# Kernel tuning notes

Hardware: AMD Instinct MI355X
Metric: run time of the kernel (lower is better)

The kernel has to match this reference:

```python
import jax, jax.numpy as jnp
import numpy as np

EPS = 1e-5  # BatchNorm eps (torch default); BN is in training mode with gamma=1, beta=0 (init values)


def bn(x, axes):
    m = jnp.mean(x, axis=axes, keepdims=True)
    v = jnp.var(x, axis=axes, keepdims=True)
    return (x - m) * jax.lax.rsqrt(v + EPS)


def knn_idx(xyz, k):
    # brute-force squared-distance matrix [B,N,N], k smallest
    d = jnp.sum((xyz[:, :, None, :] - xyz[:, None, :, :]) ** 2, axis=-1)
    _, idx = jax.lax.top_k(-d, k)
    return idx  # [B,N,k]


def gather(x, idx):
    # x: [B,N,C], idx: [B,N,k] -> [B,N,k,C]
    return jax.vmap(lambda a, i: a[i])(x, idx)


def lse(xyz, features, idx, w):
    nbr_xyz = gather(xyz, idx)                       # [B,N,k,3]
    rel = nbr_xyz - xyz[:, :, None, :]
    dist = jnp.sqrt(jnp.maximum(jnp.sum(rel ** 2, -1, keepdims=True), 1e-12))
    nbr_f = gather(features, idx)                    # [B,N,k,C]
    enc = jnp.concatenate([rel, dist, nbr_f], -1)    # [B,N,k,C+4]
    return jax.nn.relu(bn(jnp.einsum('bnkc,oc->bnko', enc, w), (0, 1, 2)))


def att_pool(x, sw1, sw2, sb2, mw):
    # x: [B,N,k,C]
    h = jax.nn.relu(bn(jnp.einsum('bnkc,oc->bnko', x, sw1), (0, 1, 2)))
    scores = jax.nn.softmax(jnp.einsum('bnkc,oc->bnko', h, sw2) + sb2, axis=2)  # softmax over k
    feat = jnp.sum(x * scores, axis=2)               # [B,N,C]
    return jax.nn.relu(bn(jnp.einsum('bnc,oc->bno', feat, mw), (0, 1)))


def drb(x, w1, w2):
    # in_channels == out_channels -> identity shortcut
    h = jax.nn.relu(bn(jnp.einsum('bnc,oc->bno', x, w1), (0, 1)))
    h = bn(jnp.einsum('bnc,oc->bno', h, w2), (0, 1))
    return jax.nn.relu(h + x)


def setup_inputs() -> dict:
    key = jax.random.key(0)
    B, N, C, K, OUT = 4, 8192, 32, 16, 128
    H = OUT // 2  # 64
    ks = jax.random.split(key, 16)
    s = 0.05
    return {
        'xyz': jax.random.normal(ks[0], (B, N, 3), jnp.float32),
        'features': jax.random.normal(ks[1], (B, N, C), jnp.float32),
        'w_lse1': jax.random.normal(ks[2], (H, C + 4), jnp.float32) * s,
        'w_lse2': jax.random.normal(ks[3], (H, C + 4), jnp.float32) * s,
        'ap1_sw1': jax.random.normal(ks[4], (H, H), jnp.float32) * s,
        'ap1_sw2': jax.random.normal(ks[5], (1, H), jnp.float32) * s,
        'ap1_sb2': jax.random.normal(ks[6], (1,), jnp.float32) * s,
        'ap1_mw': jax.random.normal(ks[7], (H, H), jnp.float32) * s,
        'ap2_sw1': jax.random.normal(ks[8], (H, H), jnp.float32) * s,
        'ap2_sw2': jax.random.normal(ks[9], (1, H), jnp.float32) * s,
        'ap2_sb2': jax.random.normal(ks[10], (1,), jnp.float32) * s,
        'ap2_mw': jax.random.normal(ks[11], (H, H), jnp.float32) * s,
        'drb_w1': jax.random.normal(ks[12], (OUT, OUT), jnp.float32) * s,
        'drb_w2': jax.random.normal(ks[13], (OUT, OUT), jnp.float32) * s,
    }


def reference(xyz, features, w_lse1, w_lse2, ap1_sw1, ap1_sw2, ap1_sb2, ap1_mw,
              ap2_sw1, ap2_sw2, ap2_sb2, ap2_mw, drb_w1, drb_w2):
    K = 16
    idx = knn_idx(xyz, K)  # original calls knn twice on same xyz -> identical indices
    f1 = att_pool(lse(xyz, features, idx, w_lse1), ap1_sw1, ap1_sw2, ap1_sb2, ap1_mw)
    f2 = att_pool(lse(xyz, features, idx, w_lse2), ap2_sw1, ap2_sw2, ap2_sb2, ap2_mw)
    agg = jnp.concatenate([f1, f2], axis=-1)  # [B,N,128]
    return drb(agg, drb_w1, drb_w2)           # [B,N,128]
```

## Files before the change

kernel.cpp:

```cpp
#include <hip/hip_runtime.h>
#include <hip/hip_bf16.h>
#include <hip/hip_fp16.h>
#include <float.h>
#include <math.h>

#define DEVFN __device__ __forceinline__

DEVFN void wavefence() { __builtin_amdgcn_wave_barrier(); }

using half8 = __attribute__((ext_vector_type(8))) _Float16;
using f32x4 = __attribute__((ext_vector_type(4))) float;

namespace {
constexpr int Bq = 4, Nq = 8192, Cq = 32, Kq = 16;
constexpr int PTS = Bq * Nq;
constexpr int CH = 16;
constexpr int CAND = Nq / CH;
constexpr double ROWS = 524288.0;

constexpr int DS_Y = 0, DS_Z = 256, DS_G = 512, DS_H1 = 768, DS_H2 = 1024;

constexpr size_t OFF_KD   = 0;
constexpr size_t OFF_KJ   = (size_t)32 << 20;
constexpr size_t OFF_X    = 0;
constexpr size_t OFF_Z    = (size_t)64 << 20;
constexpr size_t OFF_H1   = 0;
constexpr size_t OFF_H2   = (size_t)16 << 20;
constexpr size_t OFF_GRAW = (size_t)192 << 20;
constexpr size_t OFF_AGG  = (size_t)208 << 20;
constexpr size_t OFF_IDX  = (size_t)224 << 20;
constexpr size_t OFF_DST  = (size_t)226 << 20;
constexpr size_t OFF_MST  = ((size_t)226 << 20) + 10240;
constexpr size_t OFF_BNP  = ((size_t)226 << 20) + 16384;
constexpr size_t WS_NEED  = ((size_t)226 << 20) + 32768;
constexpr size_t FB_GRAW  = (size_t)64 << 20;
constexpr size_t FB_AGG   = (size_t)80 << 20;
constexpr size_t FB_H1    = (size_t)96 << 20;
constexpr size_t FB_H2    = (size_t)112 << 20;
constexpr size_t FB_IDX   = (size_t)128 << 20;
constexpr size_t FB_DST   = (size_t)130 << 20;
constexpr size_t FB_MST   = ((size_t)130 << 20) + 10240;
constexpr size_t FB_BNP   = ((size_t)130 << 20) + 16384;
}

#define TOP16_DECL                                                           \
  float e0=FLT_MAX,e1=FLT_MAX,e2=FLT_MAX,e3=FLT_MAX,e4=FLT_MAX,e5=FLT_MAX,  \
        e6=FLT_MAX,e7=FLT_MAX,e8=FLT_MAX,e9=FLT_MAX,e10=FLT_MAX,            \
        e11=FLT_MAX,e12=FLT_MAX,e13=FLT_MAX,e14=FLT_MAX,e15=FLT_MAX;

#define PMERGE(i, im1, im2)                                                  \
  e##i = fminf(fminf(e##i, fmaxf(e##im1, b0)), fmaxf(e##im2, b1));
#define PMERGE_ALL                                                           \
  PMERGE(15,14,13) PMERGE(14,13,12) PMERGE(13,12,11) PMERGE(12,11,10)        \
  PMERGE(11,10,9) PMERGE(10,9,8) PMERGE(9,8,7) PMERGE(8,7,6) PMERGE(7,6,5)   \
  PMERGE(6,5,4) PMERGE(5,4,3) PMERGE(4,3,2) PMERGE(3,2,1) PMERGE(2,1,0)      \
  e1 = fminf(fminf(e1, fmaxf(e0, b0)), b1);                                  \
  e0 = fminf(e0, b0);

DEVFN float distf(const float4 c, const float qx, const float qy, const float qz) {
  const float dx = qx - c.x, dy = qy - c.y, dz = qz - c.z;
  return __fadd_rn(__fadd_rn(__fmul_rn(dx, dx), __fmul_rn(dy, dy)), __fmul_rn(dz, dz));
}

__global__ __launch_bounds__(256, 4) void knn_chunk_kernel(const float* __restrict__ xyz,
                                                           float* __restrict__ pd,
                                                           int* __restrict__ pj) {
  const int b = blockIdx.z;
  const int ch = blockIdx.y;
  const int n = blockIdx.x * 256 + threadIdx.x;
  __shared__ __align__(16) float4 tile[CAND];
  const float* xb = xyz + (size_t)b * Nq * 3;
  for (int t = threadIdx.x; t < CAND; t += 256) {
    const int j = ch * CAND + t;
    tile[t] = make_float4(xb[j * 3], xb[j * 3 + 1], xb[j * 3 + 2], 0.f);
  }
  __syncthreads();
  const float qx = xb[n * 3], qy = xb[n * 3 + 1], qz = xb[n * 3 + 2];
  TOP16_DECL;
  for (int t = 0; t < CAND; t += 4) {
    const float4 c0 = tile[t], c1 = tile[t + 1], c2 = tile[t + 2], c3 = tile[t + 3];
    const float u0 = distf(c0, qx, qy, qz);
    const float u1 = distf(c1, qx, qy, qz);
    const float u2 = distf(c2, qx, qy, qz);
    const float u3 = distf(c3, qx, qy, qz);
    { const float b0 = fminf(u0, u1), b1 = fmaxf(u0, u1); PMERGE_ALL }
    { const float b0 = fminf(u2, u3), b1 = fmaxf(u2, u3); PMERGE_ALL }
  }
  const float kth = e15;
  const size_t base = (((size_t)b * Nq + n) * CH + ch) * Kq;
  int cnt = 0, tfirst = -1;
  for (int t = 0; t < CAND; ++t) {
    const float d = distf(tile[t], qx, qy, qz);
    if (d < kth) { pd[base + cnt] = d; pj[base + cnt] = ch * CAND + t; ++cnt; }
    tfirst = (d == kth && tfirst < 0) ? t : tfirst;
  }
  if (cnt == 15) {
    pd[base + 15] = kth; pj[base + 15] = ch * CAND + tfirst; cnt = 16;
  }
  if (__any(cnt < 16)) {
    for (int t = 0; t < CAND; ++t) {
      const float d = distf(tile[t], qx, qy, qz);
      if (d == kth && cnt < 16) { pd[base + cnt] = d; pj[base + cnt] = ch * CAND + t; ++cnt; }
    }
  }
}

__global__ __launch_bounds__(256, 4) void knn_merge_kernel(const float* __restrict__ pd,
                                                           const int* __restrict__ pj,
                                                           int* __restrict__ idxo) {
  const int q = blockIdx.x * 256 + threadIdx.x;
  const float* dp = pd + (size_t)q * CH * Kq;
  const int* jp = pj + (size_t)q * CH * Kq;
  TOP16_DECL;
  for (int t = 0; t < CH * Kq; t += 4) {
    const float4 v = *(const float4*)(dp + t);
    { const float b0 = fminf(v.x, v.y), b1 = fmaxf(v.x, v.y); PMERGE_ALL }
    { const float b0 = fminf(v.z, v.w), b1 = fmaxf(v.z, v.w); PMERGE_ALL }
  }
  const float kth = e15;
  int* op = idxo + (size_t)q * Kq;
  int cnt = 0;
  for (int t = 0; t < CH * Kq; ++t) {
    const float d = dp[t];
    if (d < kth) { op[cnt] = jp[t]; ++cnt; }
  }
  for (int t = 0; t < CH * Kq; ++t) {
    const float d = dp[t];
    if (d == kth && cnt < 16) { op[cnt] = jp[t]; ++cnt; }
  }
}

struct PF { float4 f0, f1; float nx, ny, nz; };

DEVFN PF issue_feat(const float* __restrict__ features, const float* __restrict__ xyz,
                    int p, int j, int sub) {
  const int b = p >> 13;
  const float* fr = features + ((size_t)b * Nq + j) * Cq;
  const float* xb = xyz + ((size_t)b * Nq + j) * 3;
  PF r;
  r.f0 = *(const float4*)(fr + sub * 8);
  r.f1 = *(const float4*)(fr + sub * 8 + 4);
  r.nx = xb[0]; r.ny = xb[1]; r.nz = xb[2];
  return r;
}

DEVFN int issue_idx(const int* __restrict__ idx, int p, int lane) {
  return idx[(size_t)p * Kq + (lane >> 2)];
}

DEVFN float3 issue_query(const float* __restrict__ xyz, int p) {
  const float* q = xyz + (size_t)p * 3;
  return make_float3(q[0], q[1], q[2]);
}

DEVFN void commit_enc(__half* __restrict__ enc, int lane, const PF& pf,
                      float qx, float qy, float qz) {
  const int k = lane >> 2, sub = lane & 3;
  __half* er = enc + k * 40;
  union { float4 f; __half2 h[4]; } u;
  u.h[0] = __floats2half2_rn(pf.f0.x, pf.f0.y);
  u.h[1] = __floats2half2_rn(pf.f0.z, pf.f0.w);
  u.h[2] = __floats2half2_rn(pf.f1.x, pf.f1.y);
  u.h[3] = __floats2half2_rn(pf.f1.z, pf.f1.w);
  *(float4*)(er + sub * 8) = u.f;
  if (sub == 0) {
    const float rx = pf.nx - qx, ry = pf.ny - qy, rz = pf.nz - qz;
    const float ss = rx * rx + ry * ry + rz * rz;
    const float dd = sqrtf(fmaxf(ss, 1e-12f));
    __half2* rd = (__half2*)(er + 32);
    rd[0] = __floats2half2_rn(rx, ry);
    rd[1] = __floats2half2_rn(rz, dd);
  }
}

DEVFN void commit_enc128(__half* __restrict__ enc, int lane, const PF& pf,
                         float qx, float qy, float qz) {
  const int k = lane >> 2, sub = lane & 3;
  char* base = (char*)enc + k * 128;
  union { float4 f; __half2 h[4]; } u;
  u.h[0] = __floats2half2_rn(pf.f0.x, pf.f0.y);
  u.h[1] = __floats2half2_rn(pf.f0.z, pf.f0.w);
  u.h[2] = __floats2half2_rn(pf.f1.x, pf.f1.y);
  u.h[3] = __floats2half2_rn(pf.f1.z, pf.f1.w);
  *(float4*)(base + ((sub ^ (k & 7)) * 16)) = u.f;
  if (sub == 0) {
    const float rx = pf.nx - qx, ry = pf.ny - qy, rz = pf.nz - qz;
    const float ss = rx * rx + ry * ry + rz * rz;
    const float dd = sqrtf(fmaxf(ss, 1e-12f));
    __half2* aux = (__half2*)(base + ((4 ^ (k & 7)) * 16));
    aux[0] = __floats2half2_rn(rx, ry);
    aux[1] = __floats2half2_rn(rz, dd);
  }
}

DEVFN void zero_enc_pad(__half* __restrict__ enc, int lane) {
  if (lane < 16) {
    const __half2 z2 = __floats2half2_rn(0.f, 0.f);
    __half2* pz = (__half2*)(enc + lane * 40 + 36);
    pz[0] = z2; pz[1] = z2;
  }
}

DEVFN float dot40h(const __half* __restrict__ er, const __half2* __restrict__ wh2) {
  float a0 = 0.f, a1 = 0.f, a2 = 0.f, a3 = 0.f;
#pragma unroll
  for (int r = 0; r < 5; ++r) {
    union { float4 f; __half2 h[4]; } u;
    u.f = *(const float4*)(er + r * 8);
#pragma unroll
    for (int q = 0; q < 4; ++q) {
      const __half2 xv = u.h[q];
      const __half2 wv = wh2[r * 4 + q];
      if (q & 1) {
        a2 += __low2float(xv) * __low2float(wv);
        a3 += __high2float(xv) * __high2float(wv);
      } else {
        a0 += __low2float(xv) * __low2float(wv);
        a1 += __high2float(xv) * __high2float(wv);
      }
    }
  }
  return (a0 + a1) + (a2 + a3);
}

DEVFN float dot64x(const __half* __restrict__ xr, const __half2* __restrict__ sh2) {
  float a0 = 0.f, a1 = 0.f, a2 = 0.f, a3 = 0.f;
#pragma unroll
  for (int r = 0; r < 8; ++r) {
    union { float4 f; __half2 h[4]; } u;
    u.f = *(const float4*)(xr + r * 8);
#pragma unroll
    for (int q = 0; q < 4; ++q) {
      const __half2 xv = u.h[q];
      const __half2 wv = sh2[r * 4 + q];
      if (q & 1) {
        a2 += __low2float(xv) * __low2float(wv);
        a3 += __high2float(xv) * __high2float(wv);
      } else {
        a0 += __low2float(xv) * __low2float(wv);
        a1 += __high2float(xv) * __high2float(wv);
      }
    }
  }
  return (a0 + a1) + (a2 + a3);
}

DEVFN void load_w40(const float* __restrict__ Wrow, __half2* wh2) {
#pragma unroll
  for (int c = 0; c < 16; ++c)
    wh2[c] = __floats2half2_rn(Wrow[4 + 2 * c], Wrow[5 + 2 * c]);
  wh2[16] = __floats2half2_rn(Wrow[0], Wrow[1]);
  wh2[17] = __floats2half2_rn(Wrow[2], Wrow[3]);
  wh2[18] = __floats2half2_rn(0.f, 0.f);
  wh2[19] = wh2[18];
}

DEVFN void load_b1(const float* __restrict__ W, int lane, half8* b1) {
  const int o16 = lane & 15, q = lane >> 4;
#pragma unroll
  for (int t = 0; t < 4; ++t) {
    const int o = t * 16 + o16;
#pragma unroll
    for (int ks = 0; ks < 2; ++ks) {
      half8 v;
#pragma unroll
      for (int j = 0; j < 8; ++j) {
        const int s = ks * 32 + q * 8 + j;
        float wv = 0.f;
        if (s < 36) { const int orig = (s < 32) ? (s + 4) : (s - 32); wv = W[o * 36 + orig]; }
        v[j] = (_Float16)wv;
      }
      b1[t * 2 + ks] = v;
    }
  }
}

DEVFN void load_b2(const float* __restrict__ S1, int lane, half8* b2) {
  const int o16 = lane & 15, q = lane >> 4;
#pragma unroll
  for (int t = 0; t < 4; ++t) {
    const int o = t * 16 + o16;
#pragma unroll
    for (int ks = 0; ks < 2; ++ks) {
      half8 v;
#pragma unroll
      for (int j = 0; j < 8; ++j) {
        const int c = ks * 32 + q * 8 + j;
        v[j] = (_Float16)S1[o * 64 + c];
      }
      b2[t * 2 + ks] = v;
    }
  }
}

#define GATHER_PROLOGUE                                                      \
  int p = wid;                                                               \
  int jc = issue_idx(idx, p, lane);                                          \
  PF cur = issue_feat(features, xyz, p, jc, lane & 3);                       \
  float3 qc = issue_query(xyz, p);                                           \
  int pn0 = p + nw; if (pn0 >= PTS) pn0 = p;                                 \
  int jn = issue_idx(idx, pn0, lane);                                        \
  float3 qn = issue_query(xyz, pn0);                                         \
  for (; p < PTS; p += nw) {                                                 \
    int pn = p + nw; if (pn >= PTS) pn = p;                                  \
    int pn2 = pn + nw; if (pn2 >= PTS) pn2 = pn;                             \
    PF nxt = issue_feat(features, xyz, pn, jn, lane & 3);                    \
    const int jn2 = issue_idx(idx, pn2, lane);                               \
    const float3 q2 = issue_query(xyz, pn2);                                 \
    commit_enc(enc, lane, cur, qc.x, qc.y, qc.z);                            \
    wavefence();

#define GATHER_PROLOGUE_M                                                    \
  int p = wid;                                                               \
  int jc = issue_idx(idx, p, lane);                                          \
  PF cur = issue_feat(features, xyz, p, jc, lane & 3);                       \
  float3 qc = issue_query(xyz, p);                                           \
  int pn0 = p + nw; if (pn0 >= PTS) pn0 = p;                                 \
  int jn = issue_idx(idx, pn0, lane);                                        \
  float3 qn = issue_query(xyz, pn0);                                         \
  for (; p < PTS; p += nw) {                                                 \
    int pn = p + nw; if (pn >= PTS) pn = p;                                  \
    int pn2 = pn + nw; if (pn2 >= PTS) pn2 = pn;                             \
    PF nxt = issue_feat(features, xyz, pn, jn, lane & 3);                    \
    const int jn2 = issue_idx(idx, pn2, lane);                               \
    const float3 q2 = issue_query(xyz, pn2);                                 \
    commit_enc128(enc, lane, cur, qc.x, qc.y, qc.z);                         \
    wavefence();

#define GATHER_EPILOGUE                                                      \
    wavefence();                                                             \
    cur = nxt; qc = qn; qn = q2; jn = jn2;                                   \
  }

__global__ __launch_bounds__(256) void encM_kernel(const float* __restrict__ xyz,
                                                   const float* __restrict__ features,
                                                   const int* __restrict__ idx,
                                                   float* __restrict__ mstat) {
  __shared__ __align__(16) __half encS[4][16 * 40];
  __shared__ float mred[4][36 * 37];
  const int lane = threadIdx.x & 63, wv = threadIdx.x >> 6;
  __half* enc = encS[wv];
  zero_enc_pad(enc, lane);
  wavefence();
  const int li = (lane < 36) ? lane : 0;
  float macc[36];
#pragma unroll
  for (int i = 0; i < 36; ++i) macc[i] = 0.f;
  float vacc = 0.f;
  const int wid = blockIdx.x * 4 + wv, nw = gridDim.x * 4;
  GATHER_PROLOGUE
#pragma unroll
    for (int k = 0; k < 16; ++k) {
      const __half* er = enc + k * 40;
      const float ei = __half2float(er[li]);
      vacc += ei;
#pragma unroll
      for (int r = 0; r < 5; ++r) {
        union { float4 f; __half2 h[4]; } u;
        u.f = *(const float4*)(er + r * 8);
#pragma unroll
        for (int q = 0; q < 4; ++q) {
          const int s = r * 8 + 2 * q;
          if (s < 36)     macc[s]     += ei * __low2float(u.h[q]);
          if (s + 1 < 36) macc[s + 1] += ei * __high2float(u.h[q]);
        }
      }
    }
  GATHER_EPILOGUE
  if (lane < 36) {
#pragma unroll
    for (int j = 0; j < 36; ++j) mred[wv][lane * 37 + j] = macc[j];
    mred[wv][lane * 37 + 36] = vacc;
  }
  __syncthreads();
  for (int t = threadIdx.x; t < 36 * 37; t += 256) {
    const float s = mred[0][t] + mred[1][t] + mred[2][t] + mred[3][t];
    atomicAdd(&mstat[t], s);
  }
}

__global__ void y_finalize_kernel(const float* __restrict__ mstat,
                                  const float* __restrict__ wl1,
                                  const float* __restrict__ wl2,
                                  float* __restrict__ bnp) {
  const int t = threadIdx.x;
  const int br = t >> 6, o = t & 63;
  const float* W = br ? wl2 : wl1;
  double wrow[36];
  for (int s = 0; s < 36; ++s) {
    const int orig = (s < 32) ? (s + 4) : (s - 32);
    wrow[s] = (double)W[o * 36 + orig];
  }
  double mean = 0.0, ey2 = 0.0;
  for (int i = 0; i < 36; ++i) {
    mean += wrow[i] * (double)mstat[i * 37 + 36];
    double rowacc = 0.0;
    for (int j = 0; j < 36; ++j) rowacc += wrow[j] * (double)mstat[i * 37 + j];
    ey2 += wrow[i] * rowacc;
  }
  const double invR = 1.0 / ROWS;
  mean *= invR; ey2 *= invR;
  const double var = ey2 - mean * mean;
  bnp[DS_Y + br * 64 + o] = (float)mean;
  bnp[DS_Y + 128 + br * 64 + o] = (float)(1.0 / sqrt(var + 1e-5));
}

__global__ void bn_finalize_kernel(const double* __restrict__ dstat, float* __restrict__ bnp,
                                   int base, double invc) {
  const int t = threadIdx.x;
  const double m = dstat[base + t] * invc;
  const double v = dstat[base + 128 + t] * invc - m * m;
  bnp[base + t] = (float)m;
  bnp[base + 128 + t] = (float)(1.0 / sqrt(v + 1e-5));
}

__global__ __launch_bounds__(256)
void passA_mat_kernel(const float* __restrict__ xyz,
                      const float* __restrict__ features,
                      const int* __restrict__ idx,
                      const float* __restrict__ wl1,
                      const float* __restrict__ wl2,
                      const float* __restrict__ s1a,
                      const float* __restrict__ s1b,
                      const float* __restrict__ bnp,
                      double* __restrict__ dstat,
                      __half* __restrict__ xbuf,
                      float* __restrict__ zbuf,
                      int br) {
  const float* W = br ? wl2 : wl1;
  const float* S1 = br ? s1b : s1a;
  __shared__ __align__(16) __half encS[4][16 * 64];
  __shared__ __align__(16) __half xS[4][16 * 64];
  const int lane = threadIdx.x & 63, wv = threadIdx.x >> 6;
  __half* enc = encS[wv];
  __half* xL = xS[wv];
  {
    const float4 z4 = {0.f, 0.f, 0.f, 0.f};
    ((float4*)enc)[lane] = z4;
    ((float4*)enc)[lane + 64] = z4;
  }
  wavefence();
  half8 b1[8], b2[8];
  load_b1(W, lane, b1);
  load_b2(S1, lane, b2);
  const int r16 = lane & 15, q4 = lane >> 4;
  float ym4[4], ys4[4];
#pragma unroll
  for (int t = 0; t < 4; ++t) {
    ym4[t] = bnp[DS_Y + br * 64 + t * 16 + r16];
    ys4[t] = bnp[DS_Y + 128 + br * 64 + t * 16 + r16];
  }
  float zs1a[4] = {0.f, 0.f, 0.f, 0.f}, zs2a[4] = {0.f, 0.f, 0.f, 0.f};
  const int wid = blockIdx.x * 4 + wv, nw = gridDim.x * 4;
  GATHER_PROLOGUE_M
    const char* encb = (const char*)enc + r16 * 128;
    const half8 a0 = *(const half8*)(encb + (((q4)     ^ (r16 & 7)) * 16));
    const half8 a1 = *(const half8*)(encb + (((4 + q4) ^ (r16 & 7)) * 16));
    f32x4 yt[4];
#pragma unroll
    for (int t = 0; t < 4; ++t) {
      f32x4 acc = {0.f, 0.f, 0.f, 0.f};
      acc = __builtin_amdgcn_mfma_f32_16x16x32_f16(a0, b1[t * 2], acc, 0, 0, 0);
      acc = __builtin_amdgcn_mfma_f32_16x16x32_f16(a1, b1[t * 2 + 1], acc, 0, 0, 0);
      yt[t] = acc;
    }
#pragma unroll
    for (int t = 0; t < 4; ++t) {
      const int col = t * 16 + r16;
      const int chk = col >> 3;
#pragma unroll
      for (int rr = 0; rr < 4; ++rr) {
        const int row = q4 * 4 + rr;
        float xv = (yt[t][rr] - ym4[t]) * ys4[t];
        xv = xv > 0.f ? xv : 0.f;
        *(_Float16*)((char*)xL + row * 128 + ((chk ^ (row & 7)) * 16) + (col & 7) * 2) =
            (_Float16)xv;
      }
    }
    wavefence();
    const char* xlb = (const char*)xL + r16 * 128;
    const half8 xa0 = *(const half8*)(xlb + (((q4)     ^ (r16 & 7)) * 16));
    const half8 xa1 = *(const half8*)(xlb + (((4 + q4) ^ (r16 & 7)) * 16));
#pragma unroll
    for (int it = 0; it < 2; ++it) {
      const int chunk = it * 64 + lane;
      const int row = chunk >> 3, c8 = chunk & 7;
      const float4 xv4 = *(const float4*)((const char*)xL + row * 128 + ((c8 ^ (row & 7)) * 16));
      *(float4*)((char*)xbuf + (size_t)p * 2048 + chunk * 16) = xv4;
    }
    f32x4 zt[4];
#pragma unroll
    for (int t = 0; t < 4; ++t) {
      f32x4 acc = {0.f, 0.f, 0.f, 0.f};
      acc = __builtin_amdgcn_mfma_f32_16x16x32_f16(xa0, b2[t * 2], acc, 0, 0, 0);
      acc = __builtin_amdgcn_mfma_f32_16x16x32_f16(xa1, b2[t * 2 + 1], acc, 0, 0, 0);
      zt[t] = acc;
    }
#pragma unroll
    for (int t = 0; t < 4; ++t) {
#pragma unroll
      for (int rr = 0; rr < 4; ++rr) {
        const int row = q4 * 4 + rr;
        const float zv = zt[t][rr];
        zbuf[(size_t)p * 1024 + row * 64 + t * 16 + r16] = zv;
        zs1a[t] += zv; zs2a[t] += zv * zv;
      }
    }
  GATHER_EPILOGUE
#pragma unroll
  for (int t = 0; t < 4; ++t) {
    zs1a[t] += __shfl_xor(zs1a[t], 16, 64);
    zs1a[t] += __shfl_xor(zs1a[t], 32, 64);
    zs2a[t] += __shfl_xor(zs2a[t], 16, 64);
    zs2a[t] += __shfl_xor(zs2a[t], 32, 64);
  }
  if (lane < 16) {
#pragma unroll
    for (int t = 0; t < 4; ++t) {
      atomicAdd(&dstat[DS_Z + br * 64 + t * 16 + lane], (double)zs1a[t]);
      atomicAdd(&dstat[DS_Z + 128 + br * 64 + t * 16 + lane], (double)zs2a[t]);
    }
  }
}

__global__ __launch_bounds__(256)
void passB_mat_kernel(const __half* __restrict__ xbuf,
                      const float* __restrict__ zbuf,
                      const float* __restrict__ s2,
                      const float* __restrict__ sb,
                      const float* __restrict__ mw,
                      const float* __restrict__ bnp,
                      double* __restrict__ dstat,
                      float* __restrict__ graw,
                      int br) {
  __shared__ __align__(16) __half2 mwl2[64 * 34];
  __shared__ __align__(16) float featL[4][64];
  for (int t = threadIdx.x; t < 64 * 32; t += 256) {
    const int r = t >> 5, c2 = t & 31;
    mwl2[r * 34 + c2] = __floats2half2_rn(mw[r * 64 + c2 * 2], mw[r * 64 + c2 * 2 + 1]);
  }
  __syncthreads();
  const int lane = threadIdx.x & 63, wv = threadIdx.x >> 6;
  const __half2* mrow = mwl2 + lane * 34;
  const float zm = bnp[DS_Z + br * 64 + lane];
  const float zs = bnp[DS_Z + 128 + br * 64 + lane];
  const float sw2r = s2[lane];
  const float sb2v = sb[0];
  float gs1 = 0.f, gs2 = 0.f;
  const int wid = blockIdx.x * 4 + wv, nw = gridDim.x * 4;
  for (int p = wid; p < PTS; p += nw) {
    const __half* xr = xbuf + (size_t)p * 1024 + lane;
    const float* zr = zbuf + (size_t)p * 1024 + lane;
    float xv[16], pl[16];
#pragma unroll
    for (int k = 0; k < 16; ++k) {
      xv[k] = __half2float(xr[k * 64]);
      float h = (zr[k * 64] - zm) * zs;
      h = h > 0.f ? h : 0.f;
      pl[k] = h * sw2r;
    }
#pragma unroll
    for (int off = 1; off < 64; off <<= 1) {
#pragma unroll
      for (int k = 0; k < 16; ++k) pl[k] += __shfl_xor(pl[k], off, 64);
    }
    float mx = -FLT_MAX;
#pragma unroll
    for (int k = 0; k < 16; ++k) { pl[k] += sb2v; mx = fmaxf(mx, pl[k]); }
    float se = 0.f;
#pragma unroll
    for (int k = 0; k < 16; ++k) { pl[k] = expf(pl[k] - mx); se += pl[k]; }
    const float inv = 1.f / se;
    float f = 0.f;
#pragma unroll
    for (int k = 0; k < 16; ++k) f += xv[k] * (pl[k] * inv);
    featL[wv][lane] = f;
    wavefence();
    const float* featW = &featL[wv][0];
    float g0 = 0.f, g1 = 0.f, g2 = 0.f, g3 = 0.f;
#pragma unroll
    for (int c8 = 0; c8 < 8; ++c8) {
      const float4 fa = *(const float4*)(featW + c8 * 8);
      const float4 fb = *(const float4*)(featW + c8 * 8 + 4);
      const __half2 m0 = mrow[c8 * 4 + 0];
      const __half2 m1 = mrow[c8 * 4 + 1];
      const __half2 m2 = mrow[c8 * 4 + 2];
      const __half2 m3 = mrow[c8 * 4 + 3];
      g0 += fa.x * __low2float(m0); g1 += fa.y * __high2float(m0);
      g2 += fa.z * __low2float(m1); g3 += fa.w * __high2float(m1);
      g0 += fb.x * __low2float(m2); g1 += fb.y * __high2float(m2);
      g2 += fb.z * __low2float(m3); g3 += fb.w * __high2float(m3);
    }
    const float g = (g0 + g1) + (g2 + g3);
    graw[((size_t)br * PTS + p) * 64 + lane] = g;
    gs1 += g; gs2 += g * g;
    wavefence();
  }
  atomicAdd(&dstat[DS_G + br * 64 + lane], (double)gs1);
  atomicAdd(&dstat[DS_G + 128 + br * 64 + lane], (double)gs2);
}

__global__ __launch_bounds__(256)
void passA_kernel(const float* __restrict__ xyz,
                  const float* __restrict__ features,
                  const int* __restrict__ idx,
                  const float* __restrict__ wl1,
                  const float* __restrict__ wl2,
                  const float* __restrict__ s1a,
                  const float* __restrict__ s1b,
                  const float* __restrict__ bnp,
                  double* __restrict__ dstat) {
  const int br = blockIdx.y;
  const float* W = br ? wl2 : wl1;
  const float* S1 = br ? s1b : s1a;
  __shared__ __align__(16) __half encS[4][16 * 40];
  __shared__ __align__(16) __half xS[4][16 * 64];
  const int lane = threadIdx.x & 63, wv = threadIdx.x >> 6;
  __half* enc = encS[wv];
  __half* xL = xS[wv];
  zero_enc_pad(enc, lane);
  wavefence();
  __half2 wh2[20];
  load_w40(W + lane * 36, wh2);
  __half2 sh2[32];
#pragma unroll
  for (int c = 0; c < 32; ++c)
    sh2[c] = __floats2half2_rn(S1[lane * 64 + 2 * c], S1[lane * 64 + 2 * c + 1]);
  const float ym = bnp[DS_Y + br * 64 + lane];
  const float ys = bnp[DS_Y + 128 + br * 64 + lane];
  float zs1 = 0.f, zs2 = 0.f;
  const int wid = blockIdx.x * 4 + wv, nw = gridDim.x * 4;
  GATHER_PROLOGUE
#pragma unroll
    for (int k = 0; k < 16; ++k) {
      float xv = (dot40h(enc + k * 40, wh2) - ym) * ys;
      xv = xv > 0.f ? xv : 0.f;
      xL[k * 64 + lane] = __float2half(xv);
    }
    wavefence();
#pragma unroll
    for (int k = 0; k < 16; ++k) {
      const float acc = dot64x(xL + k * 64, sh2);
      zs1 += acc; zs2 += acc * acc;
    }
  GATHER_EPILOGUE
  atomicAdd(&dstat[DS_Z + br * 64 + lane], (double)zs1);
  atomicAdd(&dstat[DS_Z + 128 + br * 64 + lane], (double)zs2);
}

__global__ __launch_bounds__(256)
void passB_kernel(const float* __restrict__ xyz,
                  const float* __restrict__ features,
                  const int* __restrict__ idx,
                  const float* __restrict__ wl1,
                  const float* __restrict__ wl2,
                  const float* __restrict__ s1a,
                  const float* __restrict__ s1b,
                  const float* __restrict__ s2a,
                  const float* __restrict__ s2b,
                  const float* __restrict__ sba,
                  const float* __restrict__ sbb,
                  const float* __restrict__ mwa,
                  const float* __restrict__ mwb,
                  const float* __restrict__ bnp,
                  double* __restrict__ dstat,
                  float* __restrict__ graw) {
  const int br = blockIdx.y;
  const float* W = br ? wl2 : wl1;
  const float* S1 = br ? s1b : s1a;
  const float* S2 = br ? s2b : s2a;
  const float* SB = br ? sbb : sba;
  const float* MW = br ? mwb : mwa;
  __shared__ __align__(16) __half2 mwl2[64 * 34];
  __shared__ __align__(16) __half encS[4][16 * 40];
  __shared__ __align__(16) __half xS[4][16 * 64];
  __shared__ __align__(16) float featL[4][64];
  for (int t = threadIdx.x; t < 64 * 32; t += 256) {
    const int r = t >> 5, c2 = t & 31;
    mwl2[r * 34 + c2] = __floats2half2_rn(MW[r * 64 + c2 * 2], MW[r * 64 + c2 * 2 + 1]);
  }
  __syncthreads();
  const int lane = threadIdx.x & 63, wv = threadIdx.x >> 6;
  __half* enc = encS[wv];
  __half* xL = xS[wv];
  zero_enc_pad(enc, lane);
  wavefence();
  const __half2* mrow = mwl2 + lane * 34;
  __half2 wh2[20];
  load_w40(W + lane * 36, wh2);
  __half2 sh2[32];
#pragma unroll
  for (int c = 0; c < 32; ++c)
    sh2[c] = __floats2half2_rn(S1[lane * 64 + 2 * c], S1[lane * 64 + 2 * c + 1]);
  const float ym = bnp[DS_Y + br * 64 + lane];
  const float ys = bnp[DS_Y + 128 + br * 64 + lane];
  const float zm = bnp[DS_Z + br * 64 + lane];
  const float zs = bnp[DS_Z + 128 + br * 64 + lane];
  const float sw2r = S2[lane];
  const float sb2v = SB[0];
  float gs1 = 0.f, gs2 = 0.f;
  const int wid = blockIdx.x * 4 + wv, nw = gridDim.x * 4;
  GATHER_PROLOGUE
#pragma unroll
    for (int k = 0; k < 16; ++k) {
      float xv = (dot40h(enc + k * 40, wh2) - ym) * ys;
      xv = xv > 0.f ? xv : 0.f;
      xL[k * 64 + lane] = __float2half(xv);
    }
    wavefence();
    float pl[16];
#pragma unroll
    for (int k = 0; k < 16; ++k) {
      float h = (dot64x(xL + k * 64, sh2) - zm) * zs;
      h = h > 0.f ? h : 0.f;
      pl[k] = h * sw2r;
    }
#pragma unroll
    for (int off = 1; off < 64; off <<= 1) {
#pragma unroll
      for (int k = 0; k < 16; ++k) pl[k] += __shfl_xor(pl[k], off, 64);
    }
    float mx = -FLT_MAX;
#pragma unroll
    for (int k = 0; k < 16; ++k) { pl[k] += sb2v; mx = fmaxf(mx, pl[k]); }
    float se = 0.f;
#pragma unroll
    for (int k = 0; k < 16; ++k) { pl[k] = expf(pl[k] - mx); se += pl[k]; }
    const float inv = 1.f / se;
    float f = 0.f;
#pragma unroll
    for (int k = 0; k < 16; ++k) f += __half2float(xL[k * 64 + lane]) * (pl[k] * inv);
    featL[wv][lane] = f;
    wavefence();
    const float* featW = &featL[wv][0];
    float g0 = 0.f, g1 = 0.f, g2 = 0.f, g3 = 0.f;
#pragma unroll
    for (int c8 = 0; c8 < 8; ++c8) {
      const float4 fa = *(const float4*)(featW + c8 * 8);
      const float4 fb = *(const float4*)(featW + c8 * 8 + 4);
      const __half2 m0 = mrow[c8 * 4 + 0];
      const __half2 m1 = mrow[c8 * 4 + 1];
      const __half2 m2 = mrow[c8 * 4 + 2];
      const __half2 m3 = mrow[c8 * 4 + 3];
      g0 += fa.x * __low2float(m0); g1 += fa.y * __high2float(m0);
      g2 += fa.z * __low2float(m1); g3 += fa.w * __high2float(m1);
      g0 += fb.x * __low2float(m2); g1 += fb.y * __high2float(m2);
      g2 += fb.z * __low2float(m3); g3 += fb.w * __high2float(m3);
    }
    const float g = (g0 + g1) + (g2 + g3);
    graw[((size_t)br * PTS + p) * 64 + lane] = g;
    gs1 += g; gs2 += g * g;
  GATHER_EPILOGUE
  atomicAdd(&dstat[DS_G + br * 64 + lane], (double)gs1);
  atomicAdd(&dstat[DS_G + 128 + br * 64 + lane], (double)gs2);
}

__global__ __launch_bounds__(256) void drb_mm_kernel(const float* __restrict__ in,
                                                     const float* __restrict__ wmat,
                                                     const float* __restrict__ bnp,
                                                     double* __restrict__ dstat,
                                                     float* __restrict__ aggout,
                                                     float* __restrict__ rowout,
                                                     int bpIn, int dsOut, int mode) {
  __shared__ __align__(16) float wlds[128 * 129];
  __shared__ __align__(16) float rowS[4][128];
  for (int t = threadIdx.x; t < 128 * 128; t += 256) wlds[(t >> 7) * 129 + (t & 127)] = wmat[t];
  __syncthreads();
  const int lane = threadIdx.x & 63, wv = threadIdx.x >> 6;
  const float m0 = bnp[bpIn + lane], s0 = bnp[bpIn + 128 + lane];
  const float m1 = bnp[bpIn + 64 + lane], s1 = bnp[bpIn + 128 + 64 + lane];
  float a1s0 = 0.f, a1s1 = 0.f, a2s0 = 0.f, a2s1 = 0.f;
  const int wid = blockIdx.x * 4 + wv, nw = gridDim.x * 4;
  for (int p = wid; p < PTS; p += nw) {
    float v0, v1;
    if (mode == 0) {
      v0 = in[(size_t)p * 64 + lane];
      v1 = in[(size_t)PTS * 64 + (size_t)p * 64 + lane];
    } else {
      v0 = in[(size_t)p * 128 + lane];
      v1 = in[(size_t)p * 128 + 64 + lane];
    }
    v0 = (v0 - m0) * s0; v0 = v0 > 0.f ? v0 : 0.f;
    v1 = (v1 - m1) * s1; v1 = v1 > 0.f ? v1 : 0.f;
    rowS[wv][lane] = v0;
    rowS[wv][64 + lane] = v1;
    if (aggout) {
      aggout[(size_t)p * 128 + lane] = v0;
      aggout[(size_t)p * 128 + 64 + lane] = v1;
    }
    wavefence();
#pragma unroll
    for (int h = 0; h < 2; ++h) {
      const int o = h * 64 + lane;
      float b0 = 0.f, b1 = 0.f, b2 = 0.f, b3 = 0.f;
#pragma unroll
      for (int c4 = 0; c4 < 32; ++c4) {
        const float4 rv = *(const float4*)(&rowS[wv][c4 * 4]);
        b0 += rv.x * wlds[o * 129 + c4 * 4 + 0];
        b1 += rv.y * wlds[o * 129 + c4 * 4 + 1];
        b2 += rv.z * wlds[o * 129 + c4 * 4 + 2];
        b3 += rv.w * wlds[o * 129 + c4 * 4 + 3];
      }
      const float acc = (b0 + b1) + (b2 + b3);
      rowout[(size_t)p * 128 + o] = acc;
      if (h == 0) { a1s0 += acc; a2s0 += acc * acc; }
      else        { a1s1 += acc; a2s1 += acc * acc; }
    }
    wavefence();
  }
  atomicAdd(&dstat[dsOut + lane], (double)a1s0);
  atomicAdd(&dstat[dsOut + 64 + lane], (double)a1s1);
  atomicAdd(&dstat[dsOut + 128 + lane], (double)a2s0);
  atomicAdd(&dstat[dsOut + 128 + 64 + lane], (double)a2s1);
}

__global__ __launch_bounds__(256) void final_kernel(const float* __restrict__ h2,
                                                    const float* __restrict__ agg,
                                                    const float* __restrict__ bnp,
                                                    float* __restrict__ out) {
  const size_t e = (size_t)blockIdx.x * 256 + threadIdx.x;
  const int ch = (int)(e & 127);
  const float m = bnp[DS_H2 + ch], s = bnp[DS_H2 + 128 + ch];
  float v = (h2[e] - m) * s + agg[e];
  out[e] = v > 0.f ? v : 0.f;
}

extern "C" void kernel_launch(void* const* d_in, const int* in_sizes, int n_in,
                              void* d_out, int out_size, void* d_ws, size_t ws_size,
                              hipStream_t stream) {
  (void)in_sizes; (void)n_in; (void)out_size;
  const float* xyz      = (const float*)d_in[0];
  const float* features = (const float*)d_in[1];
  const float* w_lse1   = (const float*)d_in[2];
  const float* w_lse2   = (const float*)d_in[3];
  const float* ap1_sw1  = (const float*)d_in[4];
  const float* ap1_sw2  = (const float*)d_in[5];
  const float* ap1_sb2  = (const float*)d_in[6];
  const float* ap1_mw   = (const float*)d_in[7];
  const float* ap2_sw1  = (const float*)d_in[8];
  const float* ap2_sw2  = (const float*)d_in[9];
  const float* ap2_sb2  = (const float*)d_in[10];
  const float* ap2_mw   = (const float*)d_in[11];
  const float* drb_w1   = (const float*)d_in[12];
  const float* drb_w2   = (const float*)d_in[13];

  char* ws = (char*)d_ws;
  const bool mat = (ws_size >= WS_NEED);

  float*  knn_d = (float*)(ws + OFF_KD);
  int*    knn_j = (int*)(ws + OFF_KJ);
  int*    idx   = (int*)(ws + (mat ? OFF_IDX : FB_IDX));
  double* dstat = (double*)(ws + (mat ? OFF_DST : FB_DST));
  float*  mstat = (float*)(ws + (mat ? OFF_MST : FB_MST));
  float*  bnp   = (float*)(ws + (mat ? OFF_BNP : FB_BNP));
  float*  graw  = (float*)(ws + (mat ? OFF_GRAW : FB_GRAW));
  float*  agg   = (float*)(ws + (mat ? OFF_AGG : FB_AGG));
  float*  h1    = (float*)(ws + (mat ? OFF_H1 : FB_H1));
  float*  h2    = (float*)(ws + (mat ? OFF_H2 : FB_H2));
  float*  out   = (float*)d_out;

  (void)hipMemsetAsync(dstat, 0, 1280 * sizeof(double) + 36 * 37 * sizeof(float), stream);

  knn_chunk_kernel<<<dim3(Nq / 256, CH, Bq), 256, 0, stream>>>(xyz, knn_d, knn_j);
  knn_merge_kernel<<<dim3(PTS / 256), 256, 0, stream>>>(knn_d, knn_j, idx);

  encM_kernel<<<dim3(1280), 256, 0, stream>>>(xyz, features, idx, mstat);
  y_finalize_kernel<<<1, 128, 0, stream>>>(mstat, w_lse1, w_lse2, bnp);

  if (mat) {
    __half* xbuf = (__half*)(ws + OFF_X);
    float*  zbuf = (float*)(ws + OFF_Z);
    for (int br = 0; br < 2; ++br) {
      passA_mat_kernel<<<dim3(1280), 256, 0, stream>>>(xyz, features, idx, w_lse1, w_lse2,
                                                       ap1_sw1, ap2_sw1, bnp, dstat,
                                                       xbuf, zbuf, br);
      bn_finalize_kernel<<<1, 128, 0, stream>>>(dstat, bnp, DS_Z, 1.0 / ROWS);
      passB_mat_kernel<<<dim3(1024), 256, 0, stream>>>(xbuf, zbuf,
                                                       br ? ap2_sw2 : ap1_sw2,
                                                       br ? ap2_sb2 : ap1_sb2,
                                                       br ? ap2_mw : ap1_mw,
                                                       bnp, dstat, graw, br);
    }
  } else {
    passA_kernel<<<dim3(640, 2), 256, 0, stream>>>(xyz, features, idx, w_lse1, w_lse2,
                                                   ap1_sw1, ap2_sw1, bnp, dstat);
    bn_finalize_kernel<<<1, 128, 0, stream>>>(dstat, bnp, DS_Z, 1.0 / ROWS);
    passB_kernel<<<dim3(512, 2), 256, 0, stream>>>(xyz, features, idx, w_lse1, w_lse2,
                                                   ap1_sw1, ap2_sw1, ap1_sw2, ap2_sw2,
                                                   ap1_sb2, ap2_sb2, ap1_mw, ap2_mw,
                                                   bnp, dstat, graw);
  }
  bn_finalize_kernel<<<1, 128, 0, stream>>>(dstat, bnp, DS_G, 1.0 / PTS);

  drb_mm_kernel<<<dim3(512), 256, 0, stream>>>(graw, drb_w1, bnp, dstat, agg, h1,
                                               DS_G, DS_H1, 0);
  bn_finalize_kernel<<<1, 128, 0, stream>>>(dstat, bnp, DS_H1, 1.0 / PTS);

  drb_mm_kernel<<<dim3(512), 256, 0, stream>>>(h1, drb_w2, bnp, dstat, nullptr, h2,
                                               DS_H1, DS_H2, 1);
  bn_finalize_kernel<<<1, 128, 0, stream>>>(dstat, bnp, DS_H2, 1.0 / PTS);

  final_kernel<<<dim3(PTS * 128 / 256), 256, 0, stream>>>(h2, agg, bnp, out);
}
```

Before: 1.458 ms.

## Replace per-pair insertion top-16 with bitonic batch-of-16 merge in KNN

The per-candidate insertion network that kept the 16 smallest distances is replaced. Candidates are now processed sixteen at a time: they are bitonic-sorted, merged against the running list with an elementwise min on the reversed batch, and the list is re-sorted with a half-cleaner. This is applied in both the chunk kernel and the merge kernel. The aim is to cut the min/max instructions spent per candidate in the brute-force neighbour search, at the cost of holding more values in registers per thread.

```diff
diff --git a/kernel.cpp b/kernel.cpp
--- a/kernel.cpp
+++ b/kernel.cpp
@@ -43,19 +43,42 @@
 constexpr size_t FB_BNP   = ((size_t)130 << 20) + 16384;
 }
 
-#define TOP16_DECL                                                           \
-  float e0=FLT_MAX,e1=FLT_MAX,e2=FLT_MAX,e3=FLT_MAX,e4=FLT_MAX,e5=FLT_MAX,  \
-        e6=FLT_MAX,e7=FLT_MAX,e8=FLT_MAX,e9=FLT_MAX,e10=FLT_MAX,            \
-        e11=FLT_MAX,e12=FLT_MAX,e13=FLT_MAX,e14=FLT_MAX,e15=FLT_MAX;
-
-#define PMERGE(i, im1, im2)                                                  \
-  e##i = fminf(fminf(e##i, fmaxf(e##im1, b0)), fmaxf(e##im2, b1));
-#define PMERGE_ALL                                                           \
-  PMERGE(15,14,13) PMERGE(14,13,12) PMERGE(13,12,11) PMERGE(12,11,10)        \
-  PMERGE(11,10,9) PMERGE(10,9,8) PMERGE(9,8,7) PMERGE(8,7,6) PMERGE(7,6,5)   \
-  PMERGE(6,5,4) PMERGE(5,4,3) PMERGE(4,3,2) PMERGE(3,2,1) PMERGE(2,1,0)      \
-  e1 = fminf(fminf(e1, fmaxf(e0, b0)), b1);                                  \
-  e0 = fminf(e0, b0);
+DEVFN void ce_asc(float& a, float& b) {
+  const float lo = fminf(a, b), hi = fmaxf(a, b);
+  a = lo; b = hi;
+}
+
+DEVFN void topk16_update(float* __restrict__ L, float* __restrict__ d) {
+#pragma unroll
+  for (int k = 2; k <= 16; k <<= 1) {
+#pragma unroll
+    for (int j = k >> 1; j > 0; j >>= 1) {
+#pragma unroll
+      for (int i = 0; i < 16; ++i) {
+        const int l = i ^ j;
+        if (l > i) {
+          if ((i & k) == 0) {
+            const float lo = fminf(d[i], d[l]), hi = fmaxf(d[i], d[l]);
+            d[i] = lo; d[l] = hi;
+          } else {
+            const float lo = fminf(d[i], d[l]), hi = fmaxf(d[i], d[l]);
+            d[i] = hi; d[l] = lo;
+          }
+        }
+      }
+    }
+  }
+#pragma unroll
+  for (int i = 0; i < 16; ++i) L[i] = fminf(L[i], d[15 - i]);
+#pragma unroll
+  for (int j = 8; j > 0; j >>= 1) {
+#pragma unroll
+    for (int i = 0; i < 16; ++i) {
+      const int l = i ^ j;
+      if (l > i) ce_asc(L[i], L[l]);
+    }
+  }
+}
 
 DEVFN float distf(const float4 c, const float qx, const float qy, const float qz) {
   const float dx = qx - c.x, dy = qy - c.y, dz = qz - c.z;
@@ -76,17 +99,16 @@
   }
   __syncthreads();
   const float qx = xb[n * 3], qy = xb[n * 3 + 1], qz = xb[n * 3 + 2];
-  TOP16_DECL;
-  for (int t = 0; t < CAND; t += 4) {
-    const float4 c0 = tile[t], c1 = tile[t + 1], c2 = tile[t + 2], c3 = tile[t + 3];
-    const float u0 = distf(c0, qx, qy, qz);
-    const float u1 = distf(c1, qx, qy, qz);
-    const float u2 = distf(c2, qx, qy, qz);
-    const float u3 = distf(c3, qx, qy, qz);
-    { const float b0 = fminf(u0, u1), b1 = fmaxf(u0, u1); PMERGE_ALL }
-    { const float b0 = fminf(u2, u3), b1 = fmaxf(u2, u3); PMERGE_ALL }
-  }
-  const float kth = e15;
+  float L[16];
+#pragma unroll
+  for (int i = 0; i < 16; ++i) L[i] = FLT_MAX;
+  for (int t = 0; t < CAND; t += 16) {
+    float d[16];
+#pragma unroll
+    for (int u = 0; u < 16; ++u) d[u] = distf(tile[t + u], qx, qy, qz);
+    topk16_update(L, d);
+  }
+  const float kth = L[15];
   const size_t base = (((size_t)b * Nq + n) * CH + ch) * Kq;
   int cnt = 0, tfirst = -1;
   for (int t = 0; t < CAND; ++t) {
@@ -111,13 +133,19 @@
   const int q = blockIdx.x * 256 + threadIdx.x;
   const float* dp = pd + (size_t)q * CH * Kq;
   const int* jp = pj + (size_t)q * CH * Kq;
-  TOP16_DECL;
-  for (int t = 0; t < CH * Kq; t += 4) {
-    const float4 v = *(const float4*)(dp + t);
-    { const float b0 = fminf(v.x, v.y), b1 = fmaxf(v.x, v.y); PMERGE_ALL }
-    { const float b0 = fminf(v.z, v.w), b1 = fmaxf(v.z, v.w); PMERGE_ALL }
-  }
-  const float kth = e15;
+  float L[16];
+#pragma unroll
+  for (int i = 0; i < 16; ++i) L[i] = FLT_MAX;
+  for (int t = 0; t < CH * Kq; t += 16) {
+    float d[16];
+#pragma unroll
+    for (int u = 0; u < 16; u += 4) {
+      const float4 v = *(const float4*)(dp + t + u);
+      d[u] = v.x; d[u + 1] = v.y; d[u + 2] = v.z; d[u + 3] = v.w;
+    }
+    topk16_update(L, d);
+  }
+  const float kth = L[15];
   int* op = idxo + (size_t)q * Kq;
   int cnt = 0;
   for (int t = 0; t < CH * Kq; ++t) {
```

Result: faster. 1.348 ms (-7.5%).
